# Kernel tuning notes

Hardware: AMD Instinct MI355X
Metric: run time of the kernel (lower is better)

Reference implementation:

```python
import jax, jax.numpy as jnp
import numpy as np
import math

B, SES, SEQ, H, K = 16, 16, 64, 512, 32
L = SES * SEQ


def setup_inputs() -> dict:
    key = jax.random.key(0)
    ks = jax.random.split(key, 16)
    s = 1.0 / math.sqrt(H)
    return {
        "user_emb": jax.random.normal(ks[0], (B, H), jnp.float32),
        "item_emb": jax.random.normal(ks[1], (B, SES, SEQ, H), jnp.float32),
        "mask": jnp.zeros((B, L, K), jnp.float32),
        "index": jax.random.randint(ks[2], (L, K), 0, L, jnp.int64),
        "Wq": jax.random.normal(ks[3], (H, H), jnp.float32) * s,
        "bq": jnp.zeros((H,), jnp.float32),
        "Wk": jax.random.normal(ks[4], (H, H), jnp.float32) * s,
        "bk": jnp.zeros((H,), jnp.float32),
        "Wv": jax.random.normal(ks[5], (H, H), jnp.float32) * s,
        "bv": jnp.zeros((H,), jnp.float32),
        "Wd": jax.random.normal(ks[6], (H, H), jnp.float32) * s,
        "bd": jnp.zeros((H,), jnp.float32),
        "ln_g": jnp.ones((H,), jnp.float32),
        "ln_b": jnp.zeros((H,), jnp.float32),
    }


def reference(user_emb, item_emb, mask, index, Wq, bq, Wk, bk, Wv, bv, Wd, bd, ln_g, ln_b):
    b, ses, seq, h = item_emb.shape
    l = ses * seq
    item_flat = item_emb.reshape(b, l, h)
    q = user_emb @ Wq.T + bq                       # [B, H]
    k = item_flat @ Wk.T + bk                      # [B, L, H]
    v = item_flat @ Wv.T + bv                      # [B, L, H]
    # scalar query against all L keys, scaled by sqrt(hidden_size)
    scores = jnp.einsum("bh,blh->bl", q, k) / math.sqrt(h)
    scores = scores[:, index] + mask               # gather -> [B, L, K]
    w = jax.nn.softmax(scores, axis=-1)            # [B, L, K]
    vg = v[:, index, :]                            # gather -> [B, L, K, H]
    attn_out = jnp.einsum("blk,blkh->blh", w, vg)  # [B, L, H]
    dense = attn_out @ Wd.T + bd
    x = dense + item_flat                          # residual (dropout = identity, eval)
    mu = jnp.mean(x, axis=-1, keepdims=True)
    var = jnp.var(x, axis=-1, keepdims=True)
    y = (x - mu) / jnp.sqrt(var + 1e-12) * ln_g + ln_b
    return y.reshape(b, ses, seq, h)
```

## Files before the change

kernel.cpp:

```cpp
#include <hip/hip_runtime.h>
#include <math.h>

constexpr int HD   = 512;
constexpr int LL   = 1024;
constexpr int MT   = 16384;
constexpr int KNBR = 32;
constexpr float SCL = 0.04419417382415922f;

typedef __attribute__((ext_vector_type(8))) short  bf16x8;
typedef __attribute__((ext_vector_type(4))) float  f32x4;

__device__ inline float b2f(unsigned short u) {
    union { unsigned int i; float f; } v; v.i = (unsigned int)u << 16; return v.f;
}
__device__ inline float b2f_lo(unsigned int u) {
    union { unsigned int i; float f; } v; v.i = u << 16; return v.f;
}
__device__ inline float b2f_hi(unsigned int u) {
    union { unsigned int i; float f; } v; v.i = u & 0xffff0000u; return v.f;
}
__device__ inline unsigned short f2b(float x) {
    union { float f; unsigned int u; } v; v.f = x;
    unsigned int r = v.u + 0x7fff + ((v.u >> 16) & 1);
    return (unsigned short)(r >> 16);
}

constexpr int PB_CONV_I = 8192;
constexpr int PB_CONV_W = 512;
constexpr int PB_Q      = 2048;

__global__ __launch_bounds__(256) void prep(
    const float* __restrict__ item, const float* __restrict__ Wv,
    const float* __restrict__ Wd, const float* __restrict__ u,
    const float* __restrict__ Wq, const float* __restrict__ bq,
    unsigned short* __restrict__ item_bf, unsigned short* __restrict__ Wv_bf,
    unsigned short* __restrict__ Wd_bf, float* __restrict__ q)
{
    const int blk = blockIdx.x, tid = threadIdx.x;

    if (blk < PB_CONV_I) {
        const int i = blk * 1024 + tid * 4;
        float4 v = *(const float4*)&item[i];
        ushort4 o;
        o.x = f2b(v.x); o.y = f2b(v.y); o.z = f2b(v.z); o.w = f2b(v.w);
        *(ushort4*)&item_bf[i] = o;
        return;
    }
    if (blk < PB_CONV_I + PB_CONV_W) {
        const int n = HD*HD;
        const int i = (blk - PB_CONV_I) * 1024 + tid * 4;
        const float* s; unsigned short* d; int off;
        if (i < n) { s = Wv; d = Wv_bf; off = i; }
        else       { s = Wd; d = Wd_bf; off = i - n; }
        float4 v = *(const float4*)&s[off];
        ushort4 o;
        o.x = f2b(v.x); o.y = f2b(v.y); o.z = f2b(v.z); o.w = f2b(v.w);
        *(ushort4*)&d[off] = o;
        return;
    }
    {
        const int wid  = (blk - PB_CONV_I - PB_CONV_W) * 4 + (tid >> 6);
        const int lane = tid & 63;
        const int b = wid >> 9, h = wid & 511;
        const float* ur = &u[b*HD + lane*8];
        const float* wr = &Wq[(size_t)h*HD + lane*8];
        const float4 u0 = *(const float4*)ur, u1 = *(const float4*)(ur+4);
        const float4 w0 = *(const float4*)wr, w1 = *(const float4*)(wr+4);
        float acc = u0.x*w0.x + u0.y*w0.y + u0.z*w0.z + u0.w*w0.w
                  + u1.x*w1.x + u1.y*w1.y + u1.z*w1.z + u1.w*w1.w;
        #pragma unroll
        for (int off = 32; off; off >>= 1) acc += __shfl_down(acc, off);
        if (lane == 0) q[b*HD + h] = acc + bq[h];
    }
}

__global__ __launch_bounds__(256) void gemm_v_r(
    const unsigned short* __restrict__ A, const unsigned short* __restrict__ W,
    const float* __restrict__ bv, const float* __restrict__ Wk,
    const float* __restrict__ bk, const float* __restrict__ q,
    unsigned short* __restrict__ v_bf, float* __restrict__ rbuf,
    float* __restrict__ s0buf)
{
    __shared__ unsigned short As[2][128 * 32];
    __shared__ unsigned short Bs[2][128 * 32];

    const int blk = blockIdx.x;
    const int tid = threadIdx.x;

    if (blk >= 512) {
        if (blk < 640) {
            __shared__ float red[4][64];
            const int rblk = blk - 512;
            const int b = rblk >> 3, c0 = (rblk & 7) * 64;
            const int cl = tid & 63, hg = tid >> 6;
            const float* qb = &q[b*HD];
            const float* wb = &Wk[(size_t)hg*128*HD + c0 + cl];
            float acc = 0.f;
            #pragma unroll 8
            for (int h = 0; h < 128; h++)
                acc += qb[hg*128 + h] * wb[(size_t)h*HD];
            red[hg][cl] = acc;
            __syncthreads();
            if (tid < 64)
                rbuf[b*HD + c0 + tid] = SCL *
                    (red[0][tid] + red[1][tid] + red[2][tid] + red[3][tid]);
        } else {
            __shared__ float sp[4];
            const int b = blk - 640;
            float p = q[b*HD + tid]*bk[tid] + q[b*HD + tid + 256]*bk[tid + 256];
            #pragma unroll
            for (int off = 32; off; off >>= 1) p += __shfl_down(p, off);
            if ((tid & 63) == 0) sp[tid >> 6] = p;
            __syncthreads();
            if (tid == 0) s0buf[b] = (sp[0] + sp[1] + sp[2] + sp[3]) * SCL;
        }
        return;
    }

    const int rowb = (blk & 7) | ((blk >> 5) << 3);
    const int colb = (blk >> 3) & 3;
    const int row0 = rowb * 128;
    const int col0 = colb * 128;

    const int wave = tid >> 6, lane = tid & 63;
    const int wm = (wave >> 1) * 64;
    const int wn = (wave & 1)  * 64;

    const int lrr = lane >> 2;
    const int cc  = lane & 3;
    int st_row[2], st_gchunk[2];
    #pragma unroll
    for (int t = 0; t < 2; t++) {
        const int m = wave*32 + t*16 + lrr;
        st_row[t]    = m;
        st_gchunk[t] = cc ^ ((m >> 1) & 3);
    }

    const int fr   = lane & 15;
    const int quad = lane >> 4;

    f32x4 acc[4][4];
    #pragma unroll
    for (int i = 0; i < 4; i++)
        #pragma unroll
        for (int j = 0; j < 4; j++)
            acc[i][j] = (f32x4){0.f, 0.f, 0.f, 0.f};

    int a_off[4], b_off[4];
    #pragma unroll
    for (int i = 0; i < 4; i++) {
        const int m = wm + i*16 + fr;
        a_off[i] = m*32 + ((quad ^ ((m >> 1) & 3)) << 3);
        const int n = wn + i*16 + fr;
        b_off[i] = n*32 + ((quad ^ ((n >> 1) & 3)) << 3);
    }

    auto stage = [&](int bf, int k0) {
        #pragma unroll
        for (int t = 0; t < 2; t++) {
            const int m = st_row[t];
            const unsigned short* ga = &A[(size_t)(row0 + m)*HD + k0 + st_gchunk[t]*8];
            __builtin_amdgcn_global_load_lds(
                (const __attribute__((address_space(1))) void*)ga,
                (__attribute__((address_space(3))) void*)&As[bf][(wave*32 + t*16)*32],
                16, 0, 0);
            const unsigned short* gw = &W[(size_t)(col0 + m)*HD + k0 + st_gchunk[t]*8];
            __builtin_amdgcn_global_load_lds(
                (const __attribute__((address_space(1))) void*)gw,
                (__attribute__((address_space(3))) void*)&Bs[bf][(wave*32 + t*16)*32],
                16, 0, 0);
        }
    };

    stage(0, 0);
    stage(1, 32);

    for (int s = 0; s < 15; ++s) {
        asm volatile("s_waitcnt vmcnt(4)" ::: "memory");
        __builtin_amdgcn_s_barrier();
        asm volatile("" ::: "memory");

        const int cur = s & 1;
        bf16x8 af[4], bfr[4];
        #pragma unroll
        for (int i = 0; i < 4; i++) {
            af[i]  = *(const bf16x8*)&As[cur][a_off[i]];
            bfr[i] = *(const bf16x8*)&Bs[cur][b_off[i]];
        }
        asm volatile("s_waitcnt lgkmcnt(0)" ::: "memory");
        __builtin_amdgcn_sched_barrier(0);
        __builtin_amdgcn_s_barrier();

        if (s + 2 < 16) stage(cur, (s + 2) * 32);

        __builtin_amdgcn_s_setprio(1);
        #pragma unroll
        for (int i = 0; i < 4; i++)
            #pragma unroll
            for (int j = 0; j < 4; j++)
                acc[i][j] = __builtin_amdgcn_mfma_f32_16x16x32_bf16(
                    af[i], bfr[j], acc[i][j], 0, 0, 0);
        __builtin_amdgcn_s_setprio(0);
    }
    {
        asm volatile("s_waitcnt vmcnt(0)" ::: "memory");
        __builtin_amdgcn_s_barrier();
        asm volatile("" ::: "memory");
        bf16x8 af[4], bfr[4];
        #pragma unroll
        for (int i = 0; i < 4; i++) {
            af[i]  = *(const bf16x8*)&As[1][a_off[i]];
            bfr[i] = *(const bf16x8*)&Bs[1][b_off[i]];
        }
        asm volatile("s_waitcnt lgkmcnt(0)" ::: "memory");
        __builtin_amdgcn_sched_barrier(0);
        #pragma unroll
        for (int i = 0; i < 4; i++)
            #pragma unroll
            for (int j = 0; j < 4; j++)
                acc[i][j] = __builtin_amdgcn_mfma_f32_16x16x32_bf16(
                    af[i], bfr[j], acc[i][j], 0, 0, 0);
    }

    #pragma unroll
    for (int j = 0; j < 4; j++) {
        const int col = col0 + wn + j*16 + fr;
        const float bb = bv[col];
        #pragma unroll
        for (int i = 0; i < 4; i++) {
            #pragma unroll
            for (int r = 0; r < 4; r++) {
                const int row = row0 + wm + i*16 + quad*4 + r;
                v_bf[(size_t)row*HD + col] = f2b(acc[i][j][r] + bb);
            }
        }
    }
}

__global__ __launch_bounds__(256) void gp_scores(
    const float* __restrict__ rbuf, const float* __restrict__ s0buf,
    const unsigned short* __restrict__ item_bf, float* __restrict__ scores)
{
    const int m = blockIdx.x * 4 + (threadIdx.x >> 6);
    const int lane = threadIdx.x & 63;
    const int b = m >> 10;
    const unsigned short* ir = &item_bf[(size_t)m*HD + lane*8];
    const uint4 iv = *(const uint4*)ir;
    const float* rr = &rbuf[b*HD + lane*8];
    const float4 r0 = *(const float4*)rr;
    const float4 r1 = *(const float4*)(rr + 4);
    float acc = r0.x*b2f_lo(iv.x) + r0.y*b2f_hi(iv.x)
              + r0.z*b2f_lo(iv.y) + r0.w*b2f_hi(iv.y)
              + r1.x*b2f_lo(iv.z) + r1.y*b2f_hi(iv.z)
              + r1.z*b2f_lo(iv.w) + r1.w*b2f_hi(iv.w);
    #pragma unroll
    for (int off = 32; off; off >>= 1) acc += __shfl_down(acc, off);
    if (lane == 0) scores[m] = acc + s0buf[b];
}

__global__ __launch_bounds__(256) void gp_attn(
    const float* __restrict__ scores, const int* __restrict__ index,
    const float* __restrict__ mask, const unsigned short* __restrict__ v,
    unsigned short* __restrict__ attn)
{
    const int bid = blockIdx.x;
    const int m = ((bid & 7) << 11) | ((bid >> 3) << 2) | (int)(threadIdx.x >> 6);
    const int lane = threadIdx.x & 63;
    const int b = m >> 10, l = m & 1023;

    const int t = lane & 31;
    const int idx = index[l*KNBR + t];
    const float s = scores[b*LL + idx] + mask[(size_t)m*KNBR + t];

    float mx = s;
    #pragma unroll
    for (int off = 16; off; off >>= 1) mx = fmaxf(mx, __shfl_xor(mx, off));
    const float e = __expf(s - mx);
    float sum = e;
    #pragma unroll
    for (int off = 16; off; off >>= 1) sum += __shfl_xor(sum, off);
    const float w = e / sum;

    const unsigned short* vb = v + (size_t)(b << 10) * HD;
    const int loff = lane * 8;
    float a[8] = {};
    #pragma unroll 8
    for (int t2 = 0; t2 < KNBR; t2++) {
        const int   it = __builtin_amdgcn_readlane(idx, t2);
        const float wt = __int_as_float(
            __builtin_amdgcn_readlane(__float_as_int(w), t2));
        const uint4 pv = *(const uint4*)(vb + (size_t)it*HD + loff);
        a[0] += wt * b2f_lo(pv.x); a[1] += wt * b2f_hi(pv.x);
        a[2] += wt * b2f_lo(pv.y); a[3] += wt * b2f_hi(pv.y);
        a[4] += wt * b2f_lo(pv.z); a[5] += wt * b2f_hi(pv.z);
        a[6] += wt * b2f_lo(pv.w); a[7] += wt * b2f_hi(pv.w);
    }
    uint4 o;
    o.x = (unsigned int)f2b(a[0]) | ((unsigned int)f2b(a[1]) << 16);
    o.y = (unsigned int)f2b(a[2]) | ((unsigned int)f2b(a[3]) << 16);
    o.z = (unsigned int)f2b(a[4]) | ((unsigned int)f2b(a[5]) << 16);
    o.w = (unsigned int)f2b(a[6]) | ((unsigned int)f2b(a[7]) << 16);
    *(uint4*)&attn[(size_t)m*HD + lane*8] = o;
}

__global__ __launch_bounds__(256) void dense_ln(
    const unsigned short* __restrict__ A,
    const unsigned short* __restrict__ W,
    const float* __restrict__ bd, const unsigned short* __restrict__ res,
    const float* __restrict__ ln_g, const float* __restrict__ ln_b,
    float* __restrict__ out)
{
    __shared__ unsigned short As[2][32 * 32];
    __shared__ unsigned short Bs[2][512 * 32];
    __shared__ float rsum[4][32], rsq[4][32];

    const int tid  = threadIdx.x;
    const int wave = tid >> 6, lane = tid & 63;
    const int row0 = blockIdx.x * 32;

    const int lrr = lane >> 2;
    const int cc  = lane & 3;
    const int fr   = lane & 15;
    const int quad = lane >> 4;

    f32x4 acc[2][8];
    #pragma unroll
    for (int i = 0; i < 2; i++)
        #pragma unroll
        for (int j = 0; j < 8; j++)
            acc[i][j] = (f32x4){0.f, 0.f, 0.f, 0.f};

    int a_off[2], b_off[8];
    #pragma unroll
    for (int i = 0; i < 2; i++) {
        const int m = i*16 + fr;
        a_off[i] = m*32 + ((quad ^ ((m >> 1) & 3)) << 3);
    }
    #pragma unroll
    for (int j = 0; j < 8; j++) {
        const int n = wave*128 + j*16 + fr;
        b_off[j] = n*32 + ((quad ^ ((n >> 1) & 3)) << 3);
    }

    auto stage = [&](int bf, int k0) {
        #pragma unroll
        for (int t = 0; t < 8; t++) {
            const int n   = wave*128 + t*16 + lrr;
            const int gch = cc ^ ((n >> 1) & 3);
            const unsigned short* gw = &W[(size_t)n*HD + k0 + gch*8];
            __builtin_amdgcn_global_load_lds(
                (const __attribute__((address_space(1))) void*)gw,
                (__attribute__((address_space(3))) void*)&Bs[bf][(wave*128 + t*16)*32],
                16, 0, 0);
        }
        if (wave < 2) {
            const int mm  = wave*16 + lrr;
            const int gch = cc ^ ((mm >> 1) & 3);
            const unsigned short* ga = &A[(size_t)(row0 + mm)*HD + k0 + gch*8];
            __builtin_amdgcn_global_load_lds(
                (const __attribute__((address_space(1))) void*)ga,
                (__attribute__((address_space(3))) void*)&As[bf][(wave*16)*32],
                16, 0, 0);
        }
    };

    stage(0, 0);
    stage(1, 32);

    for (int s = 0; s < 15; ++s) {
        if (wave < 2) asm volatile("s_waitcnt vmcnt(9)" ::: "memory");
        else          asm volatile("s_waitcnt vmcnt(8)" ::: "memory");
        __builtin_amdgcn_s_barrier();
        asm volatile("" ::: "memory");

        const int cur = s & 1;
        bf16x8 af[2], bfr[8];
        #pragma unroll
        for (int i = 0; i < 2; i++) af[i] = *(const bf16x8*)&As[cur][a_off[i]];
        #pragma unroll
        for (int j = 0; j < 8; j++) bfr[j] = *(const bf16x8*)&Bs[cur][b_off[j]];
        asm volatile("s_waitcnt lgkmcnt(0)" ::: "memory");
        __builtin_amdgcn_sched_barrier(0);
        __builtin_amdgcn_s_barrier();

        if (s + 2 < 16) stage(cur, (s + 2) * 32);

        __builtin_amdgcn_s_setprio(1);
        #pragma unroll
        for (int i = 0; i < 2; i++)
            #pragma unroll
            for (int j = 0; j < 8; j++)
                acc[i][j] = __builtin_amdgcn_mfma_f32_16x16x32_bf16(
                    af[i], bfr[j], acc[i][j], 0, 0, 0);
        __builtin_amdgcn_s_setprio(0);
    }
    {
        asm volatile("s_waitcnt vmcnt(0)" ::: "memory");
        __builtin_amdgcn_s_barrier();
        asm volatile("" ::: "memory");
        bf16x8 af[2], bfr[8];
        #pragma unroll
        for (int i = 0; i < 2; i++) af[i] = *(const bf16x8*)&As[1][a_off[i]];
        #pragma unroll
        for (int j = 0; j < 8; j++) bfr[j] = *(const bf16x8*)&Bs[1][b_off[j]];
        asm volatile("s_waitcnt lgkmcnt(0)" ::: "memory");
        __builtin_amdgcn_sched_barrier(0);
        #pragma unroll
        for (int i = 0; i < 2; i++)
            #pragma unroll
            for (int j = 0; j < 8; j++)
                acc[i][j] = __builtin_amdgcn_mfma_f32_16x16x32_bf16(
                    af[i], bfr[j], acc[i][j], 0, 0, 0);
    }
    __syncthreads();

    float bdv[8], gv[8], lbv[8];
    #pragma unroll
    for (int j = 0; j < 8; j++) {
        const int col = wave*128 + j*16 + fr;
        bdv[j] = bd[col]; gv[j] = ln_g[col]; lbv[j] = ln_b[col];
    }

    #pragma unroll
    for (int i = 0; i < 2; i++) {
        #pragma unroll
        for (int r = 0; r < 4; r++) {
            const int lrow = i*16 + quad*4 + r;
            const size_t gr = (size_t)(row0 + lrow) * HD;
            float a1 = 0.f, a2 = 0.f;
            #pragma unroll
            for (int j = 0; j < 8; j++) {
                const int col = wave*128 + j*16 + fr;
                float val = acc[i][j][r] + bdv[j] + b2f(res[gr + col]);
                acc[i][j][r] = val;
                a1 += val; a2 += val*val;
            }
            #pragma unroll
            for (int off = 1; off < 16; off <<= 1) {
                a1 += __shfl_xor(a1, off);
                a2 += __shfl_xor(a2, off);
            }
            if (fr == 0) { rsum[wave][lrow] = a1; rsq[wave][lrow] = a2; }
        }
    }
    __syncthreads();

    #pragma unroll
    for (int i = 0; i < 2; i++) {
        #pragma unroll
        for (int r = 0; r < 4; r++) {
            const int lrow = i*16 + quad*4 + r;
            const float tot  = rsum[0][lrow] + rsum[1][lrow] + rsum[2][lrow] + rsum[3][lrow];
            const float tot2 = rsq[0][lrow]  + rsq[1][lrow]  + rsq[2][lrow]  + rsq[3][lrow];
            const float mu  = tot * (1.f/HD);
            const float var = tot2 * (1.f/HD) - mu*mu;
            const float inv = rsqrtf(var + 1e-12f);
            const size_t gr = (size_t)(row0 + lrow) * HD;
            #pragma unroll
            for (int j = 0; j < 8; j++) {
                const int col = wave*128 + j*16 + fr;
                out[gr + col] = (acc[i][j][r] - mu)*inv*gv[j] + lbv[j];
            }
        }
    }
}

extern "C" void kernel_launch(void* const* d_in, const int* in_sizes, int n_in,
                              void* d_out, int out_size, void* d_ws, size_t ws_size,
                              hipStream_t stream) {
    const float* user_emb = (const float*)d_in[0];
    const float* item_emb = (const float*)d_in[1];
    const float* mask     = (const float*)d_in[2];
    const int*   index    = (const int*)  d_in[3];
    const float* Wq = (const float*)d_in[4];  const float* bq = (const float*)d_in[5];
    const float* Wk = (const float*)d_in[6];  const float* bk = (const float*)d_in[7];
    const float* Wv = (const float*)d_in[8];  const float* bv = (const float*)d_in[9];
    const float* Wd = (const float*)d_in[10]; const float* bd = (const float*)d_in[11];
    const float* ln_g = (const float*)d_in[12];
    const float* ln_b = (const float*)d_in[13];

    float* out = (float*)d_out;

    char* p = (char*)d_ws;
    unsigned short* item_bf = (unsigned short*)p; p += (size_t)MT*HD*2;
    unsigned short* v_bf    = (unsigned short*)p; p += (size_t)MT*HD*2;
    unsigned short* attn_bf = (unsigned short*)p; p += (size_t)MT*HD*2;
    unsigned short* Wv_bf   = (unsigned short*)p; p += (size_t)HD*HD*2;
    unsigned short* Wd_bf   = (unsigned short*)p; p += (size_t)HD*HD*2;
    float* q      = (float*)p; p += 16*HD*4;
    float* rbuf   = (float*)p; p += 16*HD*4;
    float* s0buf  = (float*)p; p += 16*4;
    float* scores = (float*)p; p += MT*4;

    prep<<<PB_CONV_I + PB_CONV_W + PB_Q, 256, 0, stream>>>(
        item_emb, Wv, Wd, user_emb, Wq, bq,
        item_bf, Wv_bf, Wd_bf, q);

    gemm_v_r<<<656, 256, 0, stream>>>(item_bf, Wv_bf, bv, Wk, bk, q,
                                      v_bf, rbuf, s0buf);

    gp_scores<<<MT/4, 256, 0, stream>>>(rbuf, s0buf, item_bf, scores);

    gp_attn<<<MT/4, 256, 0, stream>>>(scores, index, mask, v_bf, attn_bf);

    dense_ln<<<MT/32, 256, 0, stream>>>(attn_bf, Wd_bf, bd, item_bf,
                                        ln_g, ln_b, out);
}
```

Baseline: 183.6 us.

## Store bf16 item and weights in K-tiled layout; stage residual via LDS

```diff
diff --git a/kernel.cpp b/kernel.cpp
--- a/kernel.cpp
+++ b/kernel.cpp
@@ -33,8 +33,9 @@
     const float* __restrict__ item, const float* __restrict__ Wv,
     const float* __restrict__ Wd, const float* __restrict__ u,
     const float* __restrict__ Wq, const float* __restrict__ bq,
-    unsigned short* __restrict__ item_bf, unsigned short* __restrict__ Wv_bf,
-    unsigned short* __restrict__ Wd_bf, float* __restrict__ q)
+    unsigned short* __restrict__ item_bf, unsigned short* __restrict__ item_kt,
+    unsigned short* __restrict__ Wv_bf, unsigned short* __restrict__ Wd_bf,
+    float* __restrict__ q)
 {
     const int blk = blockIdx.x, tid = threadIdx.x;
 
@@ -44,6 +45,8 @@
         ushort4 o;
         o.x = f2b(v.x); o.y = f2b(v.y); o.z = f2b(v.z); o.w = f2b(v.w);
         *(ushort4*)&item_bf[i] = o;
+        const int m = i >> 9, k = i & 511;
+        *(ushort4*)&item_kt[((size_t)(k >> 5) * MT + m) * 32 + (k & 31)] = o;
         return;
     }
     if (blk < PB_CONV_I + PB_CONV_W) {
@@ -55,7 +58,8 @@
         float4 v = *(const float4*)&s[off];
         ushort4 o;
         o.x = f2b(v.x); o.y = f2b(v.y); o.z = f2b(v.z); o.w = f2b(v.w);
-        *(ushort4*)&d[off] = o;
+        const int nr = off >> 9, k = off & 511;
+        *(ushort4*)&d[((k >> 5) * 512 + nr) * 32 + (k & 31)] = o;
         return;
     }
     {
@@ -75,7 +79,7 @@
 }
 
 __global__ __launch_bounds__(256) void gemm_v_r(
-    const unsigned short* __restrict__ A, const unsigned short* __restrict__ W,
+    const unsigned short* __restrict__ Akt, const unsigned short* __restrict__ Wt,
     const float* __restrict__ bv, const float* __restrict__ Wk,
     const float* __restrict__ bk, const float* __restrict__ q,
     unsigned short* __restrict__ v_bf, float* __restrict__ rbuf,
@@ -155,16 +159,18 @@
         b_off[i] = n*32 + ((quad ^ ((n >> 1) & 3)) << 3);
     }
 
-    auto stage = [&](int bf, int k0) {
+    auto stage = [&](int bf, int kt) {
         #pragma unroll
         for (int t = 0; t < 2; t++) {
             const int m = st_row[t];
-            const unsigned short* ga = &A[(size_t)(row0 + m)*HD + k0 + st_gchunk[t]*8];
+            const unsigned short* ga =
+                &Akt[((size_t)kt*MT + row0 + m)*32 + st_gchunk[t]*8];
             __builtin_amdgcn_global_load_lds(
                 (const __attribute__((address_space(1))) void*)ga,
                 (__attribute__((address_space(3))) void*)&As[bf][(wave*32 + t*16)*32],
                 16, 0, 0);
-            const unsigned short* gw = &W[(size_t)(col0 + m)*HD + k0 + st_gchunk[t]*8];
+            const unsigned short* gw =
+                &Wt[((size_t)kt*512 + col0 + m)*32 + st_gchunk[t]*8];
             __builtin_amdgcn_global_load_lds(
                 (const __attribute__((address_space(1))) void*)gw,
                 (__attribute__((address_space(3))) void*)&Bs[bf][(wave*32 + t*16)*32],
@@ -173,7 +179,7 @@
     };
 
     stage(0, 0);
-    stage(1, 32);
+    stage(1, 1);
 
     for (int s = 0; s < 15; ++s) {
         asm volatile("s_waitcnt vmcnt(4)" ::: "memory");
@@ -191,7 +197,7 @@
         __builtin_amdgcn_sched_barrier(0);
         __builtin_amdgcn_s_barrier();
 
-        if (s + 2 < 16) stage(cur, (s + 2) * 32);
+        if (s + 2 < 16) stage(cur, s + 2);
 
         __builtin_amdgcn_s_setprio(1);
         #pragma unroll
@@ -305,7 +311,7 @@
 
 __global__ __launch_bounds__(256) void dense_ln(
     const unsigned short* __restrict__ A,
-    const unsigned short* __restrict__ W,
+    const unsigned short* __restrict__ Wt,
     const float* __restrict__ bd, const unsigned short* __restrict__ res,
     const float* __restrict__ ln_g, const float* __restrict__ ln_b,
     float* __restrict__ out)
@@ -342,12 +348,12 @@
         b_off[j] = n*32 + ((quad ^ ((n >> 1) & 3)) << 3);
     }
 
-    auto stage = [&](int bf, int k0) {
+    auto stage = [&](int bf, int kt) {
         #pragma unroll
         for (int t = 0; t < 8; t++) {
             const int n   = wave*128 + t*16 + lrr;
             const int gch = cc ^ ((n >> 1) & 3);
-            const unsigned short* gw = &W[(size_t)n*HD + k0 + gch*8];
+            const unsigned short* gw = &Wt[((size_t)kt*512 + n)*32 + gch*8];
             __builtin_amdgcn_global_load_lds(
                 (const __attribute__((address_space(1))) void*)gw,
                 (__attribute__((address_space(3))) void*)&Bs[bf][(wave*128 + t*16)*32],
@@ -356,7 +362,7 @@
         if (wave < 2) {
             const int mm  = wave*16 + lrr;
             const int gch = cc ^ ((mm >> 1) & 3);
-            const unsigned short* ga = &A[(size_t)(row0 + mm)*HD + k0 + gch*8];
+            const unsigned short* ga = &A[(size_t)(row0 + mm)*HD + kt*32 + gch*8];
             __builtin_amdgcn_global_load_lds(
                 (const __attribute__((address_space(1))) void*)ga,
                 (__attribute__((address_space(3))) void*)&As[bf][(wave*16)*32],
@@ -365,7 +371,7 @@
     };
 
     stage(0, 0);
-    stage(1, 32);
+    stage(1, 1);
 
     for (int s = 0; s < 15; ++s) {
         if (wave < 2) asm volatile("s_waitcnt vmcnt(9)" ::: "memory");
@@ -383,7 +389,7 @@
         __builtin_amdgcn_sched_barrier(0);
         __builtin_amdgcn_s_barrier();
 
-        if (s + 2 < 16) stage(cur, (s + 2) * 32);
+        if (s + 2 < 16) stage(cur, s + 2);
 
         __builtin_amdgcn_s_setprio(1);
         #pragma unroll
@@ -414,6 +420,16 @@
     }
     __syncthreads();
 
+    unsigned short* rs = (unsigned short*)Bs;
+    #pragma unroll
+    for (int u = 0; u < 8; u++) {
+        const int id = tid*8 + u;
+        const int rr = id >> 6, c8 = id & 63;
+        *(uint4*)&rs[rr*528 + c8*8] =
+            *(const uint4*)&res[(size_t)(row0 + rr)*HD + c8*8];
+    }
+    __syncthreads();
+
     float bdv[8], gv[8], lbv[8];
     #pragma unroll
     for (int j = 0; j < 8; j++) {
@@ -426,12 +442,11 @@
         #pragma unroll
         for (int r = 0; r < 4; r++) {
             const int lrow = i*16 + quad*4 + r;
-            const size_t gr = (size_t)(row0 + lrow) * HD;
             float a1 = 0.f, a2 = 0.f;
             #pragma unroll
             for (int j = 0; j < 8; j++) {
                 const int col = wave*128 + j*16 + fr;
-                float val = acc[i][j][r] + bdv[j] + b2f(res[gr + col]);
+                float val = acc[i][j][r] + bdv[j] + b2f(rs[lrow*528 + col]);
                 acc[i][j][r] = val;
                 a1 += val; a2 += val*val;
             }
@@ -483,6 +498,7 @@
 
     char* p = (char*)d_ws;
     unsigned short* item_bf = (unsigned short*)p; p += (size_t)MT*HD*2;
+    unsigned short* item_kt = (unsigned short*)p; p += (size_t)MT*HD*2;
     unsigned short* v_bf    = (unsigned short*)p; p += (size_t)MT*HD*2;
     unsigned short* attn_bf = (unsigned short*)p; p += (size_t)MT*HD*2;
     unsigned short* Wv_bf   = (unsigned short*)p; p += (size_t)HD*HD*2;
@@ -494,9 +510,9 @@
 
     prep<<<PB_CONV_I + PB_CONV_W + PB_Q, 256, 0, stream>>>(
         item_emb, Wv, Wd, user_emb, Wq, bq,
-        item_bf, Wv_bf, Wd_bf, q);
-
-    gemm_v_r<<<656, 256, 0, stream>>>(item_bf, Wv_bf, bv, Wk, bk, q,
+        item_bf, item_kt, Wv_bf, Wd_bf, q);
+
+    gemm_v_r<<<656, 256, 0, stream>>>(item_kt, Wv_bf, bv, Wk, bk, q,
                                       v_bf, rbuf, s0buf);
 
     gp_scores<<<MT/4, 256, 0, stream>>>(rbuf, s0buf, item_bf, scores);
```

New measurement: 178.5 us. -2.8%, faster.
